# Performance work log

Hardware: AMD Instinct MI355X
Metric: run time of the kernel (lower is better)

The kernel has to match this reference:

```python
import jax, jax.numpy as jnp
import numpy as np

B, L, D, H, K = 4, 2048, 256, 8, 32
DH = D // H
DE = 64          # d_edge
CLIP = 32        # relpos_clip


def _ln(x, g, b):
    mu = x.mean(-1, keepdims=True)
    var = ((x - mu) ** 2).mean(-1, keepdims=True)
    return (x - mu) / jnp.sqrt(var + 1e-5) * g + b


def _gelu(x):
    return jax.nn.gelu(x, approximate=False)  # torch nn.GELU default = exact erf


def _masked_softmax(logits, mask):
    logits = jnp.where(mask == 0, jnp.finfo(logits.dtype).min, logits)
    return jax.nn.softmax(logits, axis=-1)


def setup_inputs() -> dict:
    key = jax.random.key(0)
    ks = jax.random.split(key, 24)
    s = 0.02
    w = lambda i, shape: jax.random.normal(ks[i], shape, jnp.float32) * s
    p = {}
    p['x'] = jax.random.normal(ks[0], (B, L, D), jnp.float32)
    p['mask'] = jax.random.randint(ks[1], (B, L), 0, 2, jnp.int32)
    p['nbr_idx'] = jax.random.randint(ks[2], (B, L, K), 0, L, jnp.int32)
    p['nbr_mask'] = jax.random.randint(ks[3], (B, L, K), 0, 2, jnp.int32)
    p['rel_pos'] = jax.random.randint(ks[4], (B, L, K), 0, 2 * CLIP + 1, jnp.int32)
    p['g1'] = jnp.ones((D,)); p['b1'] = jnp.zeros((D,))
    p['wq'] = w(5, (D, D)); p['wk'] = w(6, (D, D)); p['wv'] = w(7, (D, D))
    p['relpos_emb'] = w(8, (2 * CLIP + 1, DE))
    p['we1'] = w(9, (DE, D)); p['be1'] = jnp.zeros((D,))
    p['we2'] = w(10, (D, 1)); p['be2'] = jnp.zeros((1,))
    p['wg1'] = w(11, (2 * D, D)); p['bg1'] = jnp.zeros((D,))
    p['wg2'] = w(12, (D, D)); p['bg2'] = jnp.zeros((D,))
    p['wlo'] = w(13, (D, D)); p['blo'] = jnp.zeros((D,))
    p['wqkv'] = w(14, (D, 3 * D)); p['wgo'] = w(15, (D, D))
    p['wf1'] = w(16, (D, D)); p['bf1'] = jnp.zeros((D,))
    p['wf2'] = w(17, (D, 2)); p['bf2'] = jnp.zeros((2,))
    p['g2'] = jnp.ones((D,)); p['b2'] = jnp.zeros((D,))
    p['wff1'] = w(18, (D, 4 * D)); p['bff1'] = jnp.zeros((4 * D,))
    p['wff2'] = w(19, (4 * D, D)); p['bff2'] = jnp.zeros((D,))
    return p


def _block(x, mask, nbr_idx, nbr_mask, rel_pos,
           g1, b1, wq, wk, wv, relpos_emb, we1, be1, we2, be2,
           wg1, bg1, wg2, bg2, wlo, blo, wqkv, wgo,
           wf1, bf1, wf2, bf2, g2, b2, wff1, bff1, wff2, bff2):
    mf = mask.astype(x.dtype)                       # [B,L]
    h = _ln(x, g1, b1)

    # ---- local graph attention (gather over K neighbors) ----
    neigh = jax.vmap(lambda hb, ib: hb[ib])(h, nbr_idx)     # [B,L,K,D]
    q = (h @ wq)[:, :, None, :]                             # [B,L,1,D]
    k = neigh @ wk                                          # [B,L,K,D]
    v = neigh @ wv
    attn = (q * k).sum(-1) / np.sqrt(D).astype(np.float32)  # [B,L,K]
    rel = jnp.clip(rel_pos, -CLIP, CLIP) + CLIP
    e = relpos_emb[rel]                                     # [B,L,K,DE]
    attn = attn + (_gelu(e @ we1 + be1) @ we2 + be2)[..., 0]
    amask = nbr_mask * mask[:, :, None]
    w = _masked_softmax(attn, amask)
    agg = jnp.einsum('blk,blkd->bld', w, v)
    agg = agg @ wlo + blo
    g = jax.nn.sigmoid(_gelu(jnp.concatenate([h, agg], -1) @ wg1 + bg1) @ wg2 + bg2)
    h_local = (h + g * agg) * mf[..., None]

    # ---- global linear attention ----
    qkv = h @ wqkv
    qg, kg, vg = jnp.split(qkv, 3, axis=-1)
    to_heads = lambda z: z.reshape(B, L, H, DH).transpose(0, 2, 1, 3)  # [B,H,L,DH]
    qg, kg, vg = to_heads(qg), to_heads(kg), to_heads(vg)
    phi = lambda z: jax.nn.elu(z) + 1.0
    qg, kg = phi(qg), phi(kg)
    m = mf[:, None, :, None]
    kg = kg * m
    vg = vg * m
    kv = jnp.einsum('bhld,bhlm->bhdm', kg, vg)
    z = 1.0 / (jnp.einsum('bhld,bhd->bhl', qg, kg.sum(axis=2)) + 1e-6)
    y = jnp.einsum('bhld,bhdm->bhlm', qg, kv) * z[..., None]
    y = y.transpose(0, 2, 1, 3).reshape(B, L, D)
    y = (y @ wgo) * mf[..., None]
    h_global = h + y

    # ---- gated fusion (softmax over 2 branches) ----
    fw = jax.nn.softmax(_gelu(h @ wf1 + bf1) @ wf2 + bf2, axis=-1)
    yc = fw[..., 0:1] * h_local + fw[..., 1:2] * h_global
    x2 = x + (yc - x)  # DropPath is identity in eval mode

    # ---- FFN ----
    hn = _ln(x2, g2, b2)
    ffn = _gelu(hn @ wff1 + bff1) @ wff2 + bff2
    out = (x2 + ffn) * mf[..., None]
    return out


def reference(x, mask, nbr_idx, nbr_mask, rel_pos,
              g1, b1, wq, wk, wv, relpos_emb, we1, be1, we2, be2,
              wg1, bg1, wg2, bg2, wlo, blo, wqkv, wgo,
              wf1, bf1, wf2, bf2, g2, b2, wff1, bff1, wff2, bff2):
    return _block(x, mask, nbr_idx, nbr_mask, rel_pos,
                  g1, b1, wq, wk, wv, relpos_emb, we1, be1, we2, be2,
                  wg1, bg1, wg2, bg2, wlo, blo, wqkv, wgo,
                  wf1, bf1, wf2, bf2, g2, b2, wff1, bff1, wff2, bff2)
```

## Files before the change

### kernel.cpp

```cpp
#include <hip/hip_runtime.h>
#include <math.h>

#define LSEQ 2048
#define BB 4
#define DD 256
#define NROWS (BB*LSEQ)
#define LDBIG 1792

typedef unsigned short u16;
typedef unsigned int u32;
typedef short s16x8 __attribute__((ext_vector_type(8)));
typedef float f32x4 __attribute__((ext_vector_type(4)));

__device__ __forceinline__ float gelu_f(float x){
    return 0.5f*x*(1.0f+erff(x*0.70710678118654752440f));
}
__device__ __forceinline__ float phi_f(float z){ return z>0.f ? z+1.f : expf(z); }
__device__ __forceinline__ float bf2f(u16 u){ union{u32 i; float f;} x; x.i = ((u32)u)<<16; return x.f; }
__device__ __forceinline__ u16 f2bf(float f){ union{float f; u32 i;} x; x.f = f; u32 r = (x.i + 0x7fff + ((x.i>>16)&1)) >> 16; return (u16)r; }

struct TransDesc { const float* src; int dstoff; int K; int N; int tstart; };
struct TransArgs { TransDesc d[11]; };

__global__ __launch_bounds__(256) void transpose_kernel(TransArgs args, u16* __restrict__ WT)
{
    int bid = blockIdx.x;
    int z = 0;
    #pragma unroll
    for (int i=1;i<11;++i) if (bid >= args.d[i].tstart) z = i;
    TransDesc e = args.d[z];
    int tid = bid - e.tstart;
    int ntx = e.N >> 5;
    int kt = tid / ntx, nt = tid - kt*ntx;
    __shared__ float tile[32][33];
    int tx = threadIdx.x & 31, ty = threadIdx.x >> 5;
    #pragma unroll
    for (int i=0;i<4;++i){
        int k = kt*32 + ty + i*8;
        tile[ty+i*8][tx] = e.src[(size_t)k*e.N + nt*32 + tx];
    }
    __syncthreads();
    #pragma unroll
    for (int i=0;i<4;++i){
        int n = nt*32 + ty + i*8;
        WT[e.dstoff + (size_t)n*e.K + kt*32 + tx] = f2bf(tile[tx][ty+i*8]);
    }
}

__global__ __launch_bounds__(256) void biasbig_kernel(const float* __restrict__ bf1, float* __restrict__ bb)
{
    int i = blockIdx.x*256 + threadIdx.x;
    bb[i] = (i >= 1536) ? bf1[i-1536] : 0.f;
}

__global__ __launch_bounds__(256) void ln_kernel(
    const float* __restrict__ x, const float* __restrict__ g,
    const float* __restrict__ b, u16* __restrict__ out)
{
    int r = blockIdx.x; int t = threadIdx.x;
    size_t i = (size_t)r*DD + t;
    float v = x[i];
    float s = v, ss = v*v;
    #pragma unroll
    for (int o=32;o>=1;o>>=1){ s += __shfl_xor(s,o); ss += __shfl_xor(ss,o); }
    __shared__ float sh[8];
    int wave = t>>6, lane = t&63;
    if (lane==0){ sh[wave]=s; sh[4+wave]=ss; }
    __syncthreads();
    float S  = sh[0]+sh[1]+sh[2]+sh[3];
    float SS = sh[4]+sh[5]+sh[6]+sh[7];
    float mu  = S*(1.f/DD);
    float var = SS*(1.f/DD) - mu*mu;
    float inv = rsqrtf(var + 1e-5f);
    out[i] = f2bf((v-mu)*inv*g[t] + b[t]);
}

template<int ACT, bool FINAL, typename CT>
__global__ __launch_bounds__(256) void mgemm(
    const u16* __restrict__ A0, const u16* __restrict__ A1, int kswitch, int lda,
    const u16* __restrict__ WT, int Kd,
    const float* __restrict__ bias, int actcol,
    CT* __restrict__ C, int ldc,
    const u16* __restrict__ addsrc, const int* __restrict__ rowmask)
{
    __shared__ u16 ldsA[4096];
    __shared__ u16 ldsB[8192];
    int t = threadIdx.x;
    int row0 = blockIdx.x*64, col0 = blockIdx.y*128;
    int l = t & 63, w = t >> 6;
    int wm = w >> 1, wn = w & 1;

    int s_ar = t >> 2, s_ao = t & 3;
    int aidx1 = (s_ar>>4)*1024 + s_ao*128 + (s_ar&15)*8;
    int aidx2 = aidx1 + 4*128;
    int s_bc = t >> 1, s_bo = (t & 1)*4;
    int bbase = (s_bc>>4)*1024 + (s_bc&15)*8;

    f32x4 acc[2][4];
    #pragma unroll
    for (int mf=0;mf<2;++mf)
        #pragma unroll
        for (int nf=0;nf<4;++nf)
            acc[mf][nf] = (f32x4){0.f,0.f,0.f,0.f};

    uint4 av1, av2, bv0, bv1, bv2, bv3;
    {
        const u16* Ab = A0; int kk = 0;
        const u16* ap = Ab + (size_t)(row0+s_ar)*lda + kk;
        av1 = *(const uint4*)(ap + s_ao*8);
        av2 = *(const uint4*)(ap + 32 + s_ao*8);
        const u16* bp = WT + (size_t)(col0 + s_bc)*Kd + s_bo*8;
        bv0 = *(const uint4*)(bp); bv1 = *(const uint4*)(bp+8);
        bv2 = *(const uint4*)(bp+16); bv3 = *(const uint4*)(bp+24);
    }

    for (int k0 = 0; k0 < Kd; k0 += 64){
        __syncthreads();
        *(uint4*)&ldsA[aidx1] = av1;
        *(uint4*)&ldsA[aidx2] = av2;
        *(uint4*)&ldsB[bbase + (s_bo  )*128] = bv0;
        *(uint4*)&ldsB[bbase + (s_bo+1)*128] = bv1;
        *(uint4*)&ldsB[bbase + (s_bo+2)*128] = bv2;
        *(uint4*)&ldsB[bbase + (s_bo+3)*128] = bv3;
        __syncthreads();
        int kn = k0 + 64;
        if (kn < Kd){
            const u16* Ab = A0; int kk = kn;
            if (kn >= kswitch){ Ab = A1; kk = kn - kswitch; }
            const u16* ap = Ab + (size_t)(row0+s_ar)*lda + kk;
            av1 = *(const uint4*)(ap + s_ao*8);
            av2 = *(const uint4*)(ap + 32 + s_ao*8);
            const u16* bp = WT + (size_t)(col0 + s_bc)*Kd + kn + s_bo*8;
            bv0 = *(const uint4*)(bp); bv1 = *(const uint4*)(bp+8);
            bv2 = *(const uint4*)(bp+16); bv3 = *(const uint4*)(bp+24);
        }
        #pragma unroll
        for (int s=0;s<2;++s){
            s16x8 af[2], bfr[4];
            #pragma unroll
            for (int mf=0;mf<2;++mf) af[mf] = *(s16x8*)&ldsA[(wm*2+mf)*1024 + (s*4+(l>>4))*128 + (l&15)*8];
            #pragma unroll
            for (int nf=0;nf<4;++nf) bfr[nf] = *(s16x8*)&ldsB[(wn*4+nf)*1024 + (s*4+(l>>4))*128 + (l&15)*8];
            #pragma unroll
            for (int mf=0; mf<2; ++mf)
                #pragma unroll
                for (int nf=0; nf<4; ++nf)
                    acc[mf][nf] = __builtin_amdgcn_mfma_f32_16x16x32_bf16(af[mf], bfr[nf], acc[mf][nf], 0,0,0);
        }
    }

    int lrow = (l>>4)*4, lcol = l&15;
    #pragma unroll
    for (int mf=0; mf<2; ++mf){
        #pragma unroll
        for (int nf=0; nf<4; ++nf){
            int col = col0 + wn*64 + nf*16 + lcol;
            float bv = bias ? bias[col] : 0.f;
            #pragma unroll
            for (int i=0;i<4;++i){
                int row = row0 + wm*32 + mf*16 + lrow + i;
                float v = acc[mf][nf][i] + bv;
                if (ACT==1){ if (col >= actcol) v = gelu_f(v); }
                else if (ACT==2) v = 1.f/(1.f+expf(-v));
                if (FINAL){
                    float mfv = (float)rowmask[row];
                    v = (bf2f(addsrc[(size_t)row*ldc + col]) + v) * mfv;
                }
                if constexpr (sizeof(CT)==2) C[(size_t)row*ldc+col] = (CT)f2bf(v);
                else                         C[(size_t)row*ldc+col] = v;
            }
        }
    }
}

__global__ __launch_bounds__(256) void bias_tab_kernel(
    const float* __restrict__ emb, const float* __restrict__ we1,
    const float* __restrict__ be1, const float* __restrict__ we2,
    const float* __restrict__ be2, float* __restrict__ tab)
{
    int r = blockIdx.x; int j = threadIdx.x;
    float acc = be1[j];
    #pragma unroll 8
    for (int d=0; d<64; ++d) acc += emb[r*64+d]*we1[d*256+j];
    float tv = gelu_f(acc)*we2[j];
    #pragma unroll
    for (int o=32;o>=1;o>>=1) tv += __shfl_xor(tv,o);
    __shared__ float sh[4];
    int wave = j>>6, lane = j&63;
    if (lane==0) sh[wave]=tv;
    __syncthreads();
    if (j==0) tab[r] = sh[0]+sh[1]+sh[2]+sh[3] + be2[0];
}

__global__ __launch_bounds__(256) void nattn_kernel(
    const u16* __restrict__ nb,
    const int* __restrict__ nbr_idx, const int* __restrict__ nbr_mask,
    const int* __restrict__ rel_pos, const int* __restrict__ mask,
    const float* __restrict__ btab, u16* __restrict__ agg)
{
    int r = blockIdx.x;
    int b = r >> 11;
    int t = threadIdx.x, lane = t&63, wave = t>>6;
    __shared__ float s_w[32];
    __shared__ float s_agg[4][256];
    uint2 qu = *(const uint2*)&nb[(size_t)r*LDBIG + lane*4];
    float q0 = bf2f(qu.x&0xffff), q1 = bf2f(qu.x>>16);
    float q2 = bf2f(qu.y&0xffff), q3 = bf2f(qu.y>>16);
    int mrow = mask[r];

    uint2 kreg[8], vreg[8];
    #pragma unroll
    for (int j=0;j<8;++j){
        int idx = nbr_idx[r*32 + wave*8 + j];
        size_t grow = ((size_t)(b<<11) + idx)*LDBIG;
        kreg[j] = *(const uint2*)&nb[grow + 256 + lane*4];
        vreg[j] = *(const uint2*)&nb[grow + 512 + lane*4];
    }
    float d[8];
    #pragma unroll
    for (int j=0;j<8;++j){
        d[j] = q0*bf2f(kreg[j].x&0xffff) + q1*bf2f(kreg[j].x>>16)
             + q2*bf2f(kreg[j].y&0xffff) + q3*bf2f(kreg[j].y>>16);
    }
    #define CMB(a,b,s) ({ float _t = (lane&(s)) ? (a) : (b); float _r = __shfl_xor(_t,(s)); (lane&(s)) ? ((b)+_r) : ((a)+_r); })
    float e10 = CMB(d[0],d[1],1), e11 = CMB(d[2],d[3],1);
    float e12 = CMB(d[4],d[5],1), e13 = CMB(d[6],d[7],1);
    float e20 = CMB(e10,e11,2),   e21 = CMB(e12,e13,2);
    float e3  = CMB(e20,e21,4);
    #undef CMB
    e3 += __shfl_xor(e3,8); e3 += __shfl_xor(e3,16); e3 += __shfl_xor(e3,32);
    if (lane < 8){
        int k = wave*8 + lane;
        int rp = rel_pos[r*32+k];
        rp = rp < -32 ? -32 : (rp > 32 ? 32 : rp);
        float logit = e3*0.0625f + btab[rp+32];
        int am = nbr_mask[r*32+k] * mrow;
        s_w[k] = am ? logit : -3.402823466e38f;
    }
    __syncthreads();
    if (wave==0){
        float lg = (lane<32) ? s_w[lane] : -3.402823466e38f;
        float m = lg;
        #pragma unroll
        for (int o=16;o>=1;o>>=1) m = fmaxf(m, __shfl_xor(m,o));
        float e = (lane<32) ? expf(lg-m) : 0.f;
        float ssum = e;
        #pragma unroll
        for (int o=16;o>=1;o>>=1) ssum += __shfl_xor(ssum,o);
        if (lane<32) s_w[lane] = e/ssum;
    }
    __syncthreads();
    float4 av = {0.f,0.f,0.f,0.f};
    #pragma unroll
    for (int j=0;j<8;++j){
        float wk = s_w[wave*8 + j];
        av.x += wk*bf2f(vreg[j].x&0xffff); av.y += wk*bf2f(vreg[j].x>>16);
        av.z += wk*bf2f(vreg[j].y&0xffff); av.w += wk*bf2f(vreg[j].y>>16);
    }
    *(float4*)&s_agg[wave][lane*4] = av;
    __syncthreads();
    float sum = s_agg[0][t]+s_agg[1][t]+s_agg[2][t]+s_agg[3][t];
    agg[(size_t)r*256 + t] = f2bf(sum);
}

__global__ __launch_bounds__(256) void linstats_kernel(
    const u16* __restrict__ qkv, const int* __restrict__ mask,
    float* __restrict__ kv, float* __restrict__ ksum)
{
    int blk = blockIdx.x;
    int bh = blk >> 4, ch = blk & 15;
    int b = bh >> 3, hh = bh & 7;
    int t = threadIdx.x;
    int d = t >> 3, m4 = (t & 7)*4;
    __shared__ float sk[8][32], sv[8][32];
    float a0=0,a1=0,a2=0,a3=0, aks=0;
    int l0 = ch*128;
    int half = t >> 7, tt = t & 127;
    int lr = tt >> 4, e2 = (tt & 15)*2;
    for (int g8=0; g8<16; ++g8){
        int l = l0 + g8*8 + lr;
        size_t base = ((size_t)b*LSEQ + l)*LDBIG + (half ? 1280 : 1024) + hh*32 + e2;
        u32 u = *(const u32*)&qkv[base];
        float mf = (float)mask[b*LSEQ + l];
        float x0 = bf2f((u16)(u & 0xffff));
        float x1 = bf2f((u16)(u >> 16));
        if (half==0){ sk[lr][e2] = phi_f(x0)*mf; sk[lr][e2+1] = phi_f(x1)*mf; }
        else        { sv[lr][e2] = x0*mf;        sv[lr][e2+1] = x1*mf; }
        __syncthreads();
        #pragma unroll
        for (int rr=0;rr<8;++rr){
            float kd = sk[rr][d];
            a0 += kd*sv[rr][m4]; a1 += kd*sv[rr][m4+1];
            a2 += kd*sv[rr][m4+2]; a3 += kd*sv[rr][m4+3];
            if ((t&7)==0) aks += kd;
        }
        __syncthreads();
    }
    size_t kb = (size_t)bh*1024 + d*32 + m4;
    atomicAdd(&kv[kb+0],a0); atomicAdd(&kv[kb+1],a1);
    atomicAdd(&kv[kb+2],a2); atomicAdd(&kv[kb+3],a3);
    if ((t&7)==0) atomicAdd(&ksum[bh*32+d], aks);
}

__global__ __launch_bounds__(256) void linapply_kernel(
    const u16* __restrict__ qkv, const float* __restrict__ kv,
    const float* __restrict__ ksum, u16* __restrict__ y)
{
    int r = blockIdx.x; int b = r >> 11;
    int t = threadIdx.x;
    __shared__ float sq[256];
    if (t < 128){
        u32 u = *(const u32*)&qkv[(size_t)r*LDBIG + 768 + t*2];
        sq[t*2]   = phi_f(bf2f((u16)(u & 0xffff)));
        sq[t*2+1] = phi_f(bf2f((u16)(u >> 16)));
    }
    __syncthreads();
    int hh = t>>5, m = t&31;
    const float* kvb = &kv[(size_t)((b<<3)+hh)*1024 + m];
    const float* ksb = &ksum[((b<<3)+hh)*32];
    const float* sqh = &sq[hh*32];
    float acc=0.f, az=0.f;
    #pragma unroll
    for (int dd=0; dd<32; ++dd){
        float qd = sqh[dd];
        acc += qd * kvb[dd*32];
        az  += qd * ksb[dd];
    }
    y[(size_t)r*256 + t] = f2bf(acc / (az + 1e-6f));
}

__global__ __launch_bounds__(64) void fw_kernel(
    const u16* __restrict__ f1, const float* __restrict__ wf2,
    const float* __restrict__ bf2, float* __restrict__ fw)
{
    int r = blockIdx.x; int lane = threadIdx.x;
    uint2 fu = *(const uint2*)&f1[(size_t)r*LDBIG + 1536 + lane*4];
    float v0 = bf2f(fu.x&0xffff), v1 = bf2f(fu.x>>16);
    float v2 = bf2f(fu.y&0xffff), v3 = bf2f(fu.y>>16);
    int dd = lane*4;
    float p0 = v0*wf2[dd*2]   + v1*wf2[dd*2+2] + v2*wf2[dd*2+4] + v3*wf2[dd*2+6];
    float p1 = v0*wf2[dd*2+1] + v1*wf2[dd*2+3] + v2*wf2[dd*2+5] + v3*wf2[dd*2+7];
    #pragma unroll
    for (int o=32;o>=1;o>>=1){ p0 += __shfl_xor(p0,o); p1 += __shfl_xor(p1,o); }
    if (lane==0){
        float a0=p0+bf2[0], a1=p1+bf2[1];
        float mx = fmaxf(a0,a1);
        float e0=expf(a0-mx), e1=expf(a1-mx);
        float s = e0+e1;
        fw[r*2] = e0/s; fw[r*2+1] = e1/s;
    }
}

__global__ __launch_bounds__(128) void combine_kernel(
    const u16* __restrict__ h, const u16* __restrict__ agglo,
    const u16* __restrict__ g, const u16* __restrict__ ygo,
    const float* __restrict__ fw, const int* __restrict__ mask,
    const float* __restrict__ g2, const float* __restrict__ b2,
    u16* __restrict__ x2, u16* __restrict__ hn)
{
    int r = blockIdx.x, t = threadIdx.x;
    size_t i = (size_t)r*DD + t*2;
    float mf = (float)mask[r];
    u32 hu = *(const u32*)&h[i],  au = *(const u32*)&agglo[i];
    u32 gu = *(const u32*)&g[i],  yu = *(const u32*)&ygo[i];
    float f0 = fw[r*2], f1v = fw[r*2+1];
    float hv0 = bf2f((u16)(hu&0xffff)), hv1 = bf2f((u16)(hu>>16));
    float ag0 = bf2f((u16)(au&0xffff)), ag1 = bf2f((u16)(au>>16));
    float gg0 = bf2f((u16)(gu&0xffff)), gg1 = bf2f((u16)(gu>>16));
    float yy0 = bf2f((u16)(yu&0xffff)), yy1 = bf2f((u16)(yu>>16));
    float v0 = f0*((hv0 + gg0*ag0)*mf) + f1v*(hv0 + yy0*mf);
    float v1 = f0*((hv1 + gg1*ag1)*mf) + f1v*(hv1 + yy1*mf);
    *(u32*)&x2[i] = (u32)f2bf(v0) | ((u32)f2bf(v1)<<16);
    float s = v0+v1, ss = v0*v0+v1*v1;
    #pragma unroll
    for (int o=32;o>=1;o>>=1){ s += __shfl_xor(s,o); ss += __shfl_xor(ss,o); }
    __shared__ float sh[4];
    int wave = t>>6, lane = t&63;
    if (lane==0){ sh[wave]=s; sh[2+wave]=ss; }
    __syncthreads();
    float S  = sh[0]+sh[1];
    float SS = sh[2]+sh[3];
    float mu  = S*(1.f/DD);
    float var = SS*(1.f/DD) - mu*mu;
    float inv = rsqrtf(var + 1e-5f);
    int j0 = t*2;
    float o0 = (v0-mu)*inv*g2[j0]   + b2[j0];
    float o1 = (v1-mu)*inv*g2[j0+1] + b2[j0+1];
    *(u32*)&hn[i] = (u32)f2bf(o0) | ((u32)f2bf(o1)<<16);
}

extern "C" void kernel_launch(void* const* d_in, const int* in_sizes, int n_in,
                              void* d_out, int out_size, void* d_ws, size_t ws_size,
                              hipStream_t stream)
{
    const float* x        = (const float*)d_in[0];
    const int*   mask     = (const int*)  d_in[1];
    const int*   nbr_idx  = (const int*)  d_in[2];
    const int*   nbr_mask = (const int*)  d_in[3];
    const int*   rel_pos  = (const int*)  d_in[4];
    const float* g1   = (const float*)d_in[5];
    const float* b1   = (const float*)d_in[6];
    const float* wq   = (const float*)d_in[7];
    const float* wk   = (const float*)d_in[8];
    const float* wv   = (const float*)d_in[9];
    const float* relpos_emb = (const float*)d_in[10];
    const float* we1  = (const float*)d_in[11];
    const float* be1  = (const float*)d_in[12];
    const float* we2  = (const float*)d_in[13];
    const float* be2  = (const float*)d_in[14];
    const float* wg1  = (const float*)d_in[15];
    const float* bg1  = (const float*)d_in[16];
    const float* wg2  = (const float*)d_in[17];
    const float* bg2  = (const float*)d_in[18];
    const float* wlo  = (const float*)d_in[19];
    const float* blo  = (const float*)d_in[20];
    const float* wqkv = (const float*)d_in[21];
    const float* wgo  = (const float*)d_in[22];
    const float* wf1  = (const float*)d_in[23];
    const float* bf1  = (const float*)d_in[24];
    const float* wf2  = (const float*)d_in[25];
    const float* bf2  = (const float*)d_in[26];
    const float* g2   = (const float*)d_in[27];
    const float* b2   = (const float*)d_in[28];
    const float* wff1 = (const float*)d_in[29];
    const float* bff1 = (const float*)d_in[30];
    const float* wff2 = (const float*)d_in[31];
    const float* bff2 = (const float*)d_in[32];
    float* out = (float*)d_out;

    unsigned char* wsb = (unsigned char*)d_ws;
    u16* bigout  = (u16*)(wsb + ((size_t)0<<20));
    u16* h_bf    = (u16*)(wsb + ((size_t)30<<20));
    u16* agg_bf  = (u16*)(wsb + ((size_t)34<<20));
    u16* agglo_bf= (u16*)(wsb + ((size_t)38<<20));
    u16* x2y_bf  = (u16*)(wsb + ((size_t)42<<20));
    u16* tg_bf   = (u16*)(wsb + ((size_t)46<<20));
    u16* ygo_bf  = (u16*)(wsb + ((size_t)50<<20));
    u16* hn_bf   = (u16*)(wsb + ((size_t)54<<20));
    u16* WT      = (u16*)(wsb + ((size_t)58<<20));
    float* btab  = (float*)(wsb + ((size_t)61<<20));
    float* bbig  = btab + 128;
    float* kvb   = bbig + 2048;
    float* ksb   = kvb + 32768;
    float* fwb   = ksb + 1024;

    const int WT_BIG  = 0;
    const int WT_LO   = 458752;
    const int WT_G1   = 524288;
    const int WT_G2   = 655360;
    const int WT_GO   = 720896;
    const int WT_FF1  = 786432;
    const int WT_FF2  = 1048576;

    TransArgs ta;
    ta.d[0]  = { wq,   WT_BIG + 0,        256,  256,    0 };
    ta.d[1]  = { wk,   WT_BIG + 65536,    256,  256,   64 };
    ta.d[2]  = { wv,   WT_BIG + 131072,   256,  256,  128 };
    ta.d[3]  = { wqkv, WT_BIG + 196608,   256,  768,  192 };
    ta.d[4]  = { wf1,  WT_BIG + 393216,   256,  256,  384 };
    ta.d[5]  = { wlo,  WT_LO,             256,  256,  448 };
    ta.d[6]  = { wg1,  WT_G1,             512,  256,  512 };
    ta.d[7]  = { wg2,  WT_G2,             256,  256,  640 };
    ta.d[8]  = { wgo,  WT_GO,             256,  256,  704 };
    ta.d[9]  = { wff1, WT_FF1,            256, 1024,  768 };
    ta.d[10] = { wff2, WT_FF2,           1024,  256, 1024 };

    const int KBIG = 1<<30;
    dim3 blk(256);

    transpose_kernel<<<1280, blk, 0, stream>>>(ta, WT);
    biasbig_kernel<<<7, blk, 0, stream>>>(bf1, bbig);
    ln_kernel<<<NROWS, blk, 0, stream>>>(x, g1, b1, h_bf);
    bias_tab_kernel<<<65, blk, 0, stream>>>(relpos_emb, we1, be1, we2, be2, btab);
    hipMemsetAsync(kvb, 0, (32768+1024)*sizeof(float), stream);
    mgemm<1,false,u16><<<dim3(128,14), blk, 0, stream>>>(h_bf, h_bf, KBIG, 256, WT+WT_BIG, 256, bbig, 1536, bigout, LDBIG, nullptr, nullptr);
    fw_kernel<<<NROWS, dim3(64), 0, stream>>>(bigout, wf2, bf2, fwb);
    linstats_kernel<<<512, blk, 0, stream>>>(bigout, mask, kvb, ksb);
    linapply_kernel<<<NROWS, blk, 0, stream>>>(bigout, kvb, ksb, x2y_bf);
    mgemm<0,false,u16><<<dim3(128,2), blk, 0, stream>>>(x2y_bf, x2y_bf, KBIG, 256, WT+WT_GO, 256, nullptr, 0, ygo_bf, 256, nullptr, nullptr);
    nattn_kernel<<<NROWS, blk, 0, stream>>>(bigout, nbr_idx, nbr_mask, rel_pos, mask, btab, agg_bf);
    mgemm<0,false,u16><<<dim3(128,2), blk, 0, stream>>>(agg_bf, agg_bf, KBIG, 256, WT+WT_LO, 256, blo, 0, agglo_bf, 256, nullptr, nullptr);
    mgemm<1,false,u16><<<dim3(128,2), blk, 0, stream>>>(h_bf, agglo_bf, 256, 256, WT+WT_G1, 512, bg1, 0, tg_bf, 256, nullptr, nullptr);
    mgemm<2,false,u16><<<dim3(128,2), blk, 0, stream>>>(tg_bf, tg_bf, KBIG, 256, WT+WT_G2, 256, bg2, 0, agg_bf, 256, nullptr, nullptr);
    combine_kernel<<<NROWS, dim3(128), 0, stream>>>(h_bf, agglo_bf, agg_bf, ygo_bf, fwb, mask, g2, b2, x2y_bf, hn_bf);
    mgemm<1,false,u16><<<dim3(128,8), blk, 0, stream>>>(hn_bf, hn_bf, KBIG, 256, WT+WT_FF1, 256, bff1, 0, bigout, 1024, nullptr, nullptr);
    mgemm<0,true,float><<<dim3(128,2), blk, 0, stream>>>(bigout, bigout, KBIG, 1024, WT+WT_FF2, 1024, bff2, 0, out, 256, x2y_bf, mask);
}
```

Measured before the change: 296.6 us.

## Merge prep kernels, batch two GEMMs, fold gate softmax into combine

Merges the weight transpose, first LayerNorm, relative-position bias table and KV-accumulator zeroing into one multi-role launch. It drops the separate bias-expansion kernel by indexing bf1 directly in the GEMM epilogue, and runs the wgo and wlo GEMMs as one launch via a z-dimension selector. The fusion-weight projection and 2-way softmax move into the combine kernel. This removes several launches and an intermediate buffer, at the cost of branchy multi-role blocks and the fw dot product being recomputed inside combine.

```diff
diff --git a/kernel.cpp b/kernel.cpp
--- a/kernel.cpp
+++ b/kernel.cpp
@@ -22,71 +22,85 @@
 struct TransDesc { const float* src; int dstoff; int K; int N; int tstart; };
 struct TransArgs { TransDesc d[11]; };
 
-__global__ __launch_bounds__(256) void transpose_kernel(TransArgs args, u16* __restrict__ WT)
+__global__ __launch_bounds__(256) void prep_kernel(
+    TransArgs args, u16* __restrict__ WT,
+    const float* __restrict__ x, const float* __restrict__ g1,
+    const float* __restrict__ b1, u16* __restrict__ h,
+    const float* __restrict__ emb, const float* __restrict__ we1,
+    const float* __restrict__ be1, const float* __restrict__ we2,
+    const float* __restrict__ be2, float* __restrict__ btab,
+    float* __restrict__ kvz)
 {
     int bid = blockIdx.x;
-    int z = 0;
-    #pragma unroll
-    for (int i=1;i<11;++i) if (bid >= args.d[i].tstart) z = i;
-    TransDesc e = args.d[z];
-    int tid = bid - e.tstart;
-    int ntx = e.N >> 5;
-    int kt = tid / ntx, nt = tid - kt*ntx;
-    __shared__ float tile[32][33];
-    int tx = threadIdx.x & 31, ty = threadIdx.x >> 5;
-    #pragma unroll
-    for (int i=0;i<4;++i){
-        int k = kt*32 + ty + i*8;
-        tile[ty+i*8][tx] = e.src[(size_t)k*e.N + nt*32 + tx];
-    }
-    __syncthreads();
-    #pragma unroll
-    for (int i=0;i<4;++i){
-        int n = nt*32 + ty + i*8;
-        WT[e.dstoff + (size_t)n*e.K + kt*32 + tx] = f2bf(tile[tx][ty+i*8]);
-    }
-}
-
-__global__ __launch_bounds__(256) void biasbig_kernel(const float* __restrict__ bf1, float* __restrict__ bb)
-{
-    int i = blockIdx.x*256 + threadIdx.x;
-    bb[i] = (i >= 1536) ? bf1[i-1536] : 0.f;
-}
-
-__global__ __launch_bounds__(256) void ln_kernel(
-    const float* __restrict__ x, const float* __restrict__ g,
-    const float* __restrict__ b, u16* __restrict__ out)
-{
-    int r = blockIdx.x; int t = threadIdx.x;
-    size_t i = (size_t)r*DD + t;
-    float v = x[i];
-    float s = v, ss = v*v;
-    #pragma unroll
-    for (int o=32;o>=1;o>>=1){ s += __shfl_xor(s,o); ss += __shfl_xor(ss,o); }
-    __shared__ float sh[8];
-    int wave = t>>6, lane = t&63;
-    if (lane==0){ sh[wave]=s; sh[4+wave]=ss; }
-    __syncthreads();
-    float S  = sh[0]+sh[1]+sh[2]+sh[3];
-    float SS = sh[4]+sh[5]+sh[6]+sh[7];
-    float mu  = S*(1.f/DD);
-    float var = SS*(1.f/DD) - mu*mu;
-    float inv = rsqrtf(var + 1e-5f);
-    out[i] = f2bf((v-mu)*inv*g[t] + b[t]);
+    if (bid < 1280){
+        int z = 0;
+        #pragma unroll
+        for (int i=1;i<11;++i) if (bid >= args.d[i].tstart) z = i;
+        TransDesc e = args.d[z];
+        int tid = bid - e.tstart;
+        int ntx = e.N >> 5;
+        int kt = tid / ntx, nt = tid - kt*ntx;
+        __shared__ float tile[32][33];
+        int tx = threadIdx.x & 31, ty = threadIdx.x >> 5;
+        #pragma unroll
+        for (int i=0;i<4;++i){
+            int k = kt*32 + ty + i*8;
+            tile[ty+i*8][tx] = e.src[(size_t)k*e.N + nt*32 + tx];
+        }
+        __syncthreads();
+        #pragma unroll
+        for (int i=0;i<4;++i){
+            int n = nt*32 + ty + i*8;
+            WT[e.dstoff + (size_t)n*e.K + kt*32 + tx] = f2bf(tile[tx][ty+i*8]);
+        }
+    } else if (bid < 9472){
+        int r = bid - 1280; int t = threadIdx.x;
+        size_t i = (size_t)r*DD + t;
+        float v = x[i];
+        float s = v, ss = v*v;
+        #pragma unroll
+        for (int o=32;o>=1;o>>=1){ s += __shfl_xor(s,o); ss += __shfl_xor(ss,o); }
+        __shared__ float sh[8];
+        int wave = t>>6, lane = t&63;
+        if (lane==0){ sh[wave]=s; sh[4+wave]=ss; }
+        __syncthreads();
+        float S  = sh[0]+sh[1]+sh[2]+sh[3];
+        float SS = sh[4]+sh[5]+sh[6]+sh[7];
+        float mu  = S*(1.f/DD);
+        float var = SS*(1.f/DD) - mu*mu;
+        float inv = rsqrtf(var + 1e-5f);
+        h[i] = f2bf((v-mu)*inv*g1[t] + b1[t]);
+    } else if (bid < 9537){
+        int r = bid - 9472; int j = threadIdx.x;
+        float acc = be1[j];
+        #pragma unroll 8
+        for (int d=0; d<64; ++d) acc += emb[r*64+d]*we1[d*256+j];
+        float tv = gelu_f(acc)*we2[j];
+        #pragma unroll
+        for (int o=32;o>=1;o>>=1) tv += __shfl_xor(tv,o);
+        __shared__ float sh2[4];
+        int wave = j>>6, lane = j&63;
+        if (lane==0) sh2[wave]=tv;
+        __syncthreads();
+        if (j==0) btab[r] = sh2[0]+sh2[1]+sh2[2]+sh2[3] + be2[0];
+    } else {
+        int idx = (bid - 9537)*256 + threadIdx.x;
+        kvz[idx] = 0.f;
+    }
 }
 
 template<int ACT, bool FINAL, typename CT>
-__global__ __launch_bounds__(256) void mgemm(
+__device__ __forceinline__ void mgemm_core(
     const u16* __restrict__ A0, const u16* __restrict__ A1, int kswitch, int lda,
     const u16* __restrict__ WT, int Kd,
     const float* __restrict__ bias, int actcol,
     CT* __restrict__ C, int ldc,
-    const u16* __restrict__ addsrc, const int* __restrict__ rowmask)
+    const u16* __restrict__ addsrc, const int* __restrict__ rowmask,
+    int row0, int col0)
 {
     __shared__ u16 ldsA[4096];
     __shared__ u16 ldsB[8192];
     int t = threadIdx.x;
-    int row0 = blockIdx.x*64, col0 = blockIdx.y*128;
     int l = t & 63, w = t >> 6;
     int wm = w >> 1, wn = w & 1;
 
@@ -105,8 +119,7 @@
 
     uint4 av1, av2, bv0, bv1, bv2, bv3;
     {
-        const u16* Ab = A0; int kk = 0;
-        const u16* ap = Ab + (size_t)(row0+s_ar)*lda + kk;
+        const u16* ap = A0 + (size_t)(row0+s_ar)*lda;
         av1 = *(const uint4*)(ap + s_ao*8);
         av2 = *(const uint4*)(ap + 32 + s_ao*8);
         const u16* bp = WT + (size_t)(col0 + s_bc)*Kd + s_bo*8;
@@ -155,7 +168,9 @@
         #pragma unroll
         for (int nf=0; nf<4; ++nf){
             int col = col0 + wn*64 + nf*16 + lcol;
-            float bv = bias ? bias[col] : 0.f;
+            float bv;
+            if (ACT==1) bv = (col >= actcol) ? bias[col-actcol] : 0.f;
+            else        bv = bias ? bias[col] : 0.f;
             #pragma unroll
             for (int i=0;i<4;++i){
                 int row = row0 + wm*32 + mf*16 + lrow + i;
@@ -173,23 +188,24 @@
     }
 }
 
-__global__ __launch_bounds__(256) void bias_tab_kernel(
-    const float* __restrict__ emb, const float* __restrict__ we1,
-    const float* __restrict__ be1, const float* __restrict__ we2,
-    const float* __restrict__ be2, float* __restrict__ tab)
-{
-    int r = blockIdx.x; int j = threadIdx.x;
-    float acc = be1[j];
-    #pragma unroll 8
-    for (int d=0; d<64; ++d) acc += emb[r*64+d]*we1[d*256+j];
-    float tv = gelu_f(acc)*we2[j];
-    #pragma unroll
-    for (int o=32;o>=1;o>>=1) tv += __shfl_xor(tv,o);
-    __shared__ float sh[4];
-    int wave = j>>6, lane = j&63;
-    if (lane==0) sh[wave]=tv;
-    __syncthreads();
-    if (j==0) tab[r] = sh[0]+sh[1]+sh[2]+sh[3] + be2[0];
+template<int ACT, bool FINAL, typename CT>
+__global__ __launch_bounds__(256) void mgemm(
+    const u16* __restrict__ A0, const u16* __restrict__ A1, int kswitch, int lda,
+    const u16* __restrict__ WT, int Kd,
+    const float* __restrict__ bias, int actcol,
+    CT* __restrict__ C, int ldc,
+    const u16* __restrict__ addsrc, const int* __restrict__ rowmask)
+{
+    mgemm_core<ACT,FINAL,CT>(A0,A1,kswitch,lda,WT,Kd,bias,actcol,C,ldc,addsrc,rowmask,
+                             blockIdx.x*64, blockIdx.y*128);
+}
+
+struct DualCfg { const u16* A; const u16* WT; const float* bias; u16* C; };
+__global__ __launch_bounds__(256) void mgemm_dual(DualCfg c0, DualCfg c1)
+{
+    DualCfg c = blockIdx.z ? c1 : c0;
+    mgemm_core<0,false,u16>(c.A, c.A, 1<<30, 256, c.WT, 256, c.bias, 0, c.C, 256,
+                            nullptr, nullptr, blockIdx.x*64, blockIdx.y*128);
 }
 
 __global__ __launch_bounds__(256) void nattn_kernel(
@@ -329,41 +345,34 @@
     y[(size_t)r*256 + t] = f2bf(acc / (az + 1e-6f));
 }
 
-__global__ __launch_bounds__(64) void fw_kernel(
-    const u16* __restrict__ f1, const float* __restrict__ wf2,
-    const float* __restrict__ bf2, float* __restrict__ fw)
-{
-    int r = blockIdx.x; int lane = threadIdx.x;
-    uint2 fu = *(const uint2*)&f1[(size_t)r*LDBIG + 1536 + lane*4];
-    float v0 = bf2f(fu.x&0xffff), v1 = bf2f(fu.x>>16);
-    float v2 = bf2f(fu.y&0xffff), v3 = bf2f(fu.y>>16);
-    int dd = lane*4;
-    float p0 = v0*wf2[dd*2]   + v1*wf2[dd*2+2] + v2*wf2[dd*2+4] + v3*wf2[dd*2+6];
-    float p1 = v0*wf2[dd*2+1] + v1*wf2[dd*2+3] + v2*wf2[dd*2+5] + v3*wf2[dd*2+7];
-    #pragma unroll
-    for (int o=32;o>=1;o>>=1){ p0 += __shfl_xor(p0,o); p1 += __shfl_xor(p1,o); }
-    if (lane==0){
-        float a0=p0+bf2[0], a1=p1+bf2[1];
-        float mx = fmaxf(a0,a1);
-        float e0=expf(a0-mx), e1=expf(a1-mx);
-        float s = e0+e1;
-        fw[r*2] = e0/s; fw[r*2+1] = e1/s;
-    }
-}
-
 __global__ __launch_bounds__(128) void combine_kernel(
     const u16* __restrict__ h, const u16* __restrict__ agglo,
     const u16* __restrict__ g, const u16* __restrict__ ygo,
-    const float* __restrict__ fw, const int* __restrict__ mask,
+    const u16* __restrict__ bigout, const float* __restrict__ wf2,
+    const float* __restrict__ bf2v, const int* __restrict__ mask,
     const float* __restrict__ g2, const float* __restrict__ b2,
     u16* __restrict__ x2, u16* __restrict__ hn)
 {
     int r = blockIdx.x, t = threadIdx.x;
+    int wave = t>>6, lane = t&63;
+    u32 fu = *(const u32*)&bigout[(size_t)r*LDBIG + 1536 + t*2];
+    float fa = bf2f((u16)(fu&0xffff)), fb = bf2f((u16)(fu>>16));
+    int dd = t*2;
+    float p0 = fa*wf2[dd*2]   + fb*wf2[dd*2+2];
+    float p1 = fa*wf2[dd*2+1] + fb*wf2[dd*2+3];
+    #pragma unroll
+    for (int o=32;o>=1;o>>=1){ p0 += __shfl_xor(p0,o); p1 += __shfl_xor(p1,o); }
+    __shared__ float shp[4];
+    if (lane==0){ shp[wave]=p0; shp[2+wave]=p1; }
+    __syncthreads();
+    float P0 = shp[0]+shp[1]+bf2v[0], P1 = shp[2]+shp[3]+bf2v[1];
+    float mx = fmaxf(P0,P1);
+    float e0 = expf(P0-mx), e1 = expf(P1-mx);
+    float f0 = e0/(e0+e1), f1v = e1/(e0+e1);
     size_t i = (size_t)r*DD + t*2;
     float mf = (float)mask[r];
     u32 hu = *(const u32*)&h[i],  au = *(const u32*)&agglo[i];
     u32 gu = *(const u32*)&g[i],  yu = *(const u32*)&ygo[i];
-    float f0 = fw[r*2], f1v = fw[r*2+1];
     float hv0 = bf2f((u16)(hu&0xffff)), hv1 = bf2f((u16)(hu>>16));
     float ag0 = bf2f((u16)(au&0xffff)), ag1 = bf2f((u16)(au>>16));
     float gg0 = bf2f((u16)(gu&0xffff)), gg1 = bf2f((u16)(gu>>16));
@@ -375,7 +384,6 @@
     #pragma unroll
     for (int o=32;o>=1;o>>=1){ s += __shfl_xor(s,o); ss += __shfl_xor(ss,o); }
     __shared__ float sh[4];
-    int wave = t>>6, lane = t&63;
     if (lane==0){ sh[wave]=s; sh[2+wave]=ss; }
     __syncthreads();
     float S  = sh[0]+sh[1];
@@ -439,10 +447,8 @@
     u16* hn_bf   = (u16*)(wsb + ((size_t)54<<20));
     u16* WT      = (u16*)(wsb + ((size_t)58<<20));
     float* btab  = (float*)(wsb + ((size_t)61<<20));
-    float* bbig  = btab + 128;
-    float* kvb   = bbig + 2048;
+    float* kvb   = btab + 128;
     float* ksb   = kvb + 32768;
-    float* fwb   = ksb + 1024;
 
     const int WT_BIG  = 0;
     const int WT_LO   = 458752;
@@ -468,21 +474,20 @@
     const int KBIG = 1<<30;
     dim3 blk(256);
 
-    transpose_kernel<<<1280, blk, 0, stream>>>(ta, WT);
-    biasbig_kernel<<<7, blk, 0, stream>>>(bf1, bbig);
-    ln_kernel<<<NROWS, blk, 0, stream>>>(x, g1, b1, h_bf);
-    bias_tab_kernel<<<65, blk, 0, stream>>>(relpos_emb, we1, be1, we2, be2, btab);
-    hipMemsetAsync(kvb, 0, (32768+1024)*sizeof(float), stream);
-    mgemm<1,false,u16><<<dim3(128,14), blk, 0, stream>>>(h_bf, h_bf, KBIG, 256, WT+WT_BIG, 256, bbig, 1536, bigout, LDBIG, nullptr, nullptr);
-    fw_kernel<<<NROWS, dim3(64), 0, stream>>>(bigout, wf2, bf2, fwb);
+    prep_kernel<<<9669, blk, 0, stream>>>(ta, WT, x, g1, b1, h_bf,
+                                          relpos_emb, we1, be1, we2, be2, btab, kvb);
+    mgemm<1,false,u16><<<dim3(128,14), blk, 0, stream>>>(h_bf, h_bf, KBIG, 256, WT+WT_BIG, 256, bf1, 1536, bigout, LDBIG, nullptr, nullptr);
     linstats_kernel<<<512, blk, 0, stream>>>(bigout, mask, kvb, ksb);
     linapply_kernel<<<NROWS, blk, 0, stream>>>(bigout, kvb, ksb, x2y_bf);
-    mgemm<0,false,u16><<<dim3(128,2), blk, 0, stream>>>(x2y_bf, x2y_bf, KBIG, 256, WT+WT_GO, 256, nullptr, 0, ygo_bf, 256, nullptr, nullptr);
     nattn_kernel<<<NROWS, blk, 0, stream>>>(bigout, nbr_idx, nbr_mask, rel_pos, mask, btab, agg_bf);
-    mgemm<0,false,u16><<<dim3(128,2), blk, 0, stream>>>(agg_bf, agg_bf, KBIG, 256, WT+WT_LO, 256, blo, 0, agglo_bf, 256, nullptr, nullptr);
+    {
+        DualCfg cgo = { x2y_bf, WT+WT_GO, nullptr, ygo_bf };
+        DualCfg clo = { agg_bf, WT+WT_LO, blo,     agglo_bf };
+        mgemm_dual<<<dim3(128,2,2), blk, 0, stream>>>(cgo, clo);
+    }
     mgemm<1,false,u16><<<dim3(128,2), blk, 0, stream>>>(h_bf, agglo_bf, 256, 256, WT+WT_G1, 512, bg1, 0, tg_bf, 256, nullptr, nullptr);
     mgemm<2,false,u16><<<dim3(128,2), blk, 0, stream>>>(tg_bf, tg_bf, KBIG, 256, WT+WT_G2, 256, bg2, 0, agg_bf, 256, nullptr, nullptr);
-    combine_kernel<<<NROWS, dim3(128), 0, stream>>>(h_bf, agglo_bf, agg_bf, ygo_bf, fwb, mask, g2, b2, x2y_bf, hn_bf);
+    combine_kernel<<<NROWS, dim3(128), 0, stream>>>(h_bf, agglo_bf, agg_bf, ygo_bf, bigout, wf2, bf2, mask, g2, b2, x2y_bf, hn_bf);
     mgemm<1,false,u16><<<dim3(128,8), blk, 0, stream>>>(hn_bf, hn_bf, KBIG, 256, WT+WT_FF1, 256, bff1, 0, bigout, 1024, nullptr, nullptr);
     mgemm<0,true,float><<<dim3(128,2), blk, 0, stream>>>(bigout, bigout, KBIG, 1024, WT+WT_FF2, 1024, bff2, 0, out, 256, x2y_bf, mask);
 }
```

New measurement: 277.6 us. -6.4%, faster.
